# Optimization experiments

Hardware: AMD Instinct MI355X
Metric: run time of the kernel (lower is better)

Reference implementation:

```python
import jax, jax.numpy as jnp
import numpy as np

N_A, N_P = 100000, 150000
N = N_A + N_P          # total nodes in concatenated feature matrix
D = 128                # emb_dim == hidden
C = 16                 # num_classes
E = 2000000            # nnz per relation


def setup_inputs() -> dict:
    key = jax.random.key(0)
    ks = jax.random.split(key, 16)
    s = 1.0 / np.sqrt(D)
    # coefficients as in init_coe: uniform(-b, b) then L1-normalized, coe_num = 1+2+2 = 5
    bound = np.sqrt(3.0 / 5)
    coe_np = np.random.RandomState(0).uniform(-bound, bound, 5)
    coe_np = coe_np / np.sum(np.abs(coe_np))
    return {
        "x0": jax.random.normal(ks[0], (N_A, D), jnp.float32),
        "x1": jax.random.normal(ks[1], (N_P, D), jnp.float32),
        "vals_ap": jax.random.uniform(ks[2], (E,), jnp.float32) * 0.01,
        "vals_pa": jax.random.uniform(ks[3], (E,), jnp.float32) * 0.01,
        # AP: rows are A nodes [0, N_A), cols are P nodes [N_A, N)
        "rows_ap": jax.random.randint(ks[4], (E,), 0, N_A, jnp.int32),
        "cols_ap": jax.random.randint(ks[5], (E,), N_A, N, jnp.int32),
        # PA: rows are P nodes [N_A, N), cols are A nodes [0, N_A)
        "rows_pa": jax.random.randint(ks[6], (E,), N_A, N, jnp.int32),
        "cols_pa": jax.random.randint(ks[7], (E,), 0, N_A, jnp.int32),
        "Wp0": jax.random.normal(ks[8], (D, D), jnp.float32) * s,
        "Wp1": jax.random.normal(ks[9], (D, D), jnp.float32) * s,
        "W1": jax.random.normal(ks[10], (D, D), jnp.float32) * s,
        "b1": jnp.zeros((D,), jnp.float32),
        "W2": jax.random.normal(ks[11], (D, C), jnp.float32) * s,
        "b2": jnp.zeros((C,), jnp.float32),
        "coe": jnp.asarray(coe_np, jnp.float32),
    }


def _spmm(rows, cols, vals, h):
    # sparse [N,N] @ dense [N,D] via gather + segment-sum
    return jax.ops.segment_sum(vals[:, None] * h[cols], rows, num_segments=N)


def _normalize(x):
    mean = x.mean(axis=1, keepdims=True)
    std = jnp.std(x, axis=1, keepdims=True, ddof=1)  # torch std is unbiased
    z = (x - mean) / std
    return jnp.where(jnp.isnan(z), 0.0, z)


def _power_pass(x, coe, ap, pa, first_order):
    # first_order: tuple of relation names in hop-1 order ("AP","PA") or ("PA","AP")
    rel = {"AP": ap, "PA": pa}
    res = coe[0] * x
    h = {}
    for ci, r in enumerate(first_order):
        h[r] = _spmm(*rel[r], x)
        res = res + coe[1 + ci] * h[r]
    # hop 2: compose relation j[:2] with previous result j[2:]
    second = [r + first_order[1 - i] for i, r in enumerate(first_order)]
    for ci, j in enumerate(second):
        out = _spmm(*rel[j[:2]], h[j[2:]])
        res = res + coe[3 + ci] * out
    return res


def reference(x0, x1, vals_ap, vals_pa, rows_ap, cols_ap, rows_pa, cols_pa,
              Wp0, Wp1, W1, b1, W2, b2, coe):
    ap = (rows_ap, cols_ap, vals_ap)
    pa = (rows_pa, cols_pa, vals_pa)
    # per-type projection then concat along node axis
    x = jnp.concatenate([x0 @ Wp0, x1 @ Wp1], axis=0)  # [N, D]
    x = jax.nn.relu(x @ W1 + b1)
    x = _normalize(x)
    # pass 1: lis = {1: [AP, PA], 2: [APPA, PAAP]}
    x = _power_pass(x, coe, ap, pa, ("AP", "PA"))
    # pass 2 (transposed series): lis_t = {1: [PA, AP], 2: [PAAP, APPA]}
    res = _power_pass(x, coe, ap, pa, ("PA", "AP"))
    return res @ W2 + b2  # [N, C]
```

## Files before the change

### kernel.cpp

```cpp
#include <hip/hip_runtime.h>
#include <hip/hip_bf16.h>


typedef float f32x2 __attribute__((ext_vector_type(2)));
typedef float f32x4 __attribute__((ext_vector_type(4)));
typedef short bf16x8 __attribute__((ext_vector_type(8)));

__device__ inline unsigned short f2bf(float x) {
    unsigned b = __float_as_uint(x);
    unsigned r = (b + 0x7fffu + ((b >> 16) & 1u)) >> 16;
    return (unsigned short)r;
}
__device__ inline float bflo(unsigned u) { return __uint_as_float(u << 16); }
__device__ inline float bfhi(unsigned u) { return __uint_as_float(u & 0xffff0000u); }

__device__ inline unsigned pk_fp8x4(float a, float b, float c, float d) {
    int v = __builtin_amdgcn_cvt_pk_fp8_f32(a, b, 0, false);
    v = __builtin_amdgcn_cvt_pk_fp8_f32(c, d, v, true);
    return (unsigned)v;
}

__global__ __launch_bounds__(128) void fuse_w(const float* __restrict__ Wp0,
                                              const float* __restrict__ Wp1,
                                              const float* __restrict__ W1,
                                              unsigned short* __restrict__ Mt0,
                                              unsigned short* __restrict__ Mt1) {
    int m = blockIdx.x >> 7;
    int i = blockIdx.x & 127;
    const float* Wp = m ? Wp1 : Wp0;
    unsigned short* Mt = m ? Mt1 : Mt0;
    __shared__ float r[128];
    int t = threadIdx.x;
    r[t] = Wp[i * 128 + t];
    __syncthreads();
    float acc = 0.f;
    #pragma unroll 8
    for (int k = 0; k < 128; ++k) acc += r[k] * W1[k * 128 + t];
    Mt[t * 128 + i] = f2bf(acc);
}

__global__ __launch_bounds__(256) void gemm_relu_norm(const float* __restrict__ xin,
                                                      const unsigned short* __restrict__ Mt,
                                                      const float* __restrict__ b1,
                                                      unsigned short* __restrict__ xbf,
                                                      unsigned char* __restrict__ x8,
                                                      int nrows) {
    __shared__ char xsh[64 * 256];
    __shared__ char xsl[64 * 256];
    __shared__ char mts[128 * 256];
    int t = threadIdx.x;
    long row0 = (long)blockIdx.x * 64;
    int rows_this = nrows - (int)row0;
    if (rows_this > 64) rows_this = 64;

    #pragma unroll
    for (int it = 0; it < 4; ++it) {
        int idx = it * 256 + t;
        int row = idx >> 4, slot = idx & 15;
        float4 v0 = {0.f, 0.f, 0.f, 0.f}, v1 = {0.f, 0.f, 0.f, 0.f};
        if (row < rows_this) {
            v0 = *(const float4*)(xin + (row0 + row) * 128 + slot * 8);
            v1 = *(const float4*)(xin + (row0 + row) * 128 + slot * 8 + 4);
        }
        float vv[8] = {v0.x, v0.y, v0.z, v0.w, v1.x, v1.y, v1.z, v1.w};
        unsigned hw[8], lw[8];
        #pragma unroll
        for (int j = 0; j < 8; ++j) {
            unsigned h = f2bf(vv[j]);
            float hv = __uint_as_float(h << 16);
            hw[j] = h;
            lw[j] = f2bf(vv[j] - hv);
        }
        uint4 ph, pl;
        ph.x = hw[0] | (hw[1] << 16); ph.y = hw[2] | (hw[3] << 16);
        ph.z = hw[4] | (hw[5] << 16); ph.w = hw[6] | (hw[7] << 16);
        pl.x = lw[0] | (lw[1] << 16); pl.y = lw[2] | (lw[3] << 16);
        pl.z = lw[4] | (lw[5] << 16); pl.w = lw[6] | (lw[7] << 16);
        int off = row * 256 + ((slot ^ (row & 7)) << 4);
        *(uint4*)&xsh[off] = ph;
        *(uint4*)&xsl[off] = pl;
    }
    #pragma unroll
    for (int it = 0; it < 8; ++it) {
        int idx = it * 256 + t;
        int row = idx >> 4, slot = idx & 15;
        uint4 mv = ((const uint4*)Mt)[idx];
        *(uint4*)&mts[row * 256 + ((slot ^ (row & 7)) << 4)] = mv;
    }
    __syncthreads();

    int w = t >> 6;
    int lidx = t & 15;
    int grp = (t >> 4) & 3;
    f32x4 acc[8];
    #pragma unroll
    for (int nt = 0; nt < 8; ++nt) acc[nt] = (f32x4){0.f, 0.f, 0.f, 0.f};

    #pragma unroll
    for (int ks = 0; ks < 4; ++ks) {
        int arow = w * 16 + lidx;
        int slot = ks * 4 + grp;
        bf16x8 ah = *(bf16x8*)&xsh[arow * 256 + ((slot ^ (arow & 7)) << 4)];
        bf16x8 al = *(bf16x8*)&xsl[arow * 256 + ((slot ^ (arow & 7)) << 4)];
        #pragma unroll
        for (int nt = 0; nt < 8; ++nt) {
            int brow = nt * 16 + lidx;
            bf16x8 bb = *(bf16x8*)&mts[brow * 256 + ((slot ^ (brow & 7)) << 4)];
            acc[nt] = __builtin_amdgcn_mfma_f32_16x16x32_bf16(al, bb, acc[nt], 0, 0, 0);
            acc[nt] = __builtin_amdgcn_mfma_f32_16x16x32_bf16(ah, bb, acc[nt], 0, 0, 0);
        }
    }

    float bias[8];
    #pragma unroll
    for (int nt = 0; nt < 8; ++nt) bias[nt] = b1[nt * 16 + lidx];

    #pragma unroll
    for (int r = 0; r < 4; ++r) {
        int row_loc = w * 16 + grp * 4 + r;
        float v[8];
        float s = 0.f;
        #pragma unroll
        for (int nt = 0; nt < 8; ++nt) {
            float x = acc[nt][r] + bias[nt];
            x = x > 0.f ? x : 0.f;
            v[nt] = x;
            s += x;
        }
        s += __shfl_xor(s, 1); s += __shfl_xor(s, 2);
        s += __shfl_xor(s, 4); s += __shfl_xor(s, 8);
        float mean = s * (1.0f / 128.0f);
        float q = 0.f;
        #pragma unroll
        for (int nt = 0; nt < 8; ++nt) {
            float d = v[nt] - mean;
            v[nt] = d;
            q += d * d;
        }
        q += __shfl_xor(q, 1); q += __shfl_xor(q, 2);
        q += __shfl_xor(q, 4); q += __shfl_xor(q, 8);
        float inv = 0.f;
        if (q > 0.f) inv = 1.0f / sqrtf(q * (1.0f / 127.0f));
        #pragma unroll
        for (int nt = 0; nt < 8; ++nt)
            *(unsigned short*)&xsh[row_loc * 256 + (nt * 16 + lidx) * 2] = f2bf(v[nt] * inv);
    }
    __syncthreads();

    #pragma unroll
    for (int it = 0; it < 4; ++it) {
        int idx = it * 256 + t;
        int row = idx >> 4, slot = idx & 15;
        if (row < rows_this) {
            uint4 zv = *(uint4*)&xsh[row * 256 + slot * 16];
            *(uint4*)(xbf + (row0 + row) * 128 + slot * 8) = zv;
            uint2 p8;
            p8.x = pk_fp8x4(bflo(zv.x), bfhi(zv.x), bflo(zv.y), bfhi(zv.y));
            p8.y = pk_fp8x4(bflo(zv.z), bfhi(zv.z), bflo(zv.w), bfhi(zv.w));
            *(uint2*)(x8 + (row0 + row) * 128 + slot * 8) = p8;
        }
    }
}

__global__ __launch_bounds__(256) void count_rows(const int* __restrict__ rows, int E,
                                                  int* __restrict__ cnt) {
    int i = (blockIdx.x * 256 + threadIdx.x) * 4;
    if (i + 4 <= E) {
        int4 r = *(const int4*)(rows + i);
        atomicAdd(&cnt[r.x], 1);
        atomicAdd(&cnt[r.y], 1);
        atomicAdd(&cnt[r.z], 1);
        atomicAdd(&cnt[r.w], 1);
    } else {
        for (; i < E; ++i) atomicAdd(&cnt[rows[i]], 1);
    }
}

__global__ __launch_bounds__(256) void scan1(const int* __restrict__ cnt, int R,
                                             int* __restrict__ rp, int* __restrict__ bt) {
    __shared__ int lds[256];
    int t = threadIdx.x, b = blockIdx.x;
    int base = b * 4096 + t * 16;
    int v[16];
    int s = 0;
    #pragma unroll
    for (int i = 0; i < 16; ++i) {
        int idx = base + i;
        int c = (idx < R) ? cnt[idx] : 0;
        v[i] = s;
        s += c;
    }
    lds[t] = s;
    __syncthreads();
    for (int off = 1; off < 256; off <<= 1) {
        int x = (t >= off) ? lds[t - off] : 0;
        __syncthreads();
        lds[t] += x;
        __syncthreads();
    }
    int excl = lds[t] - s;
    #pragma unroll
    for (int i = 0; i < 16; ++i) {
        int idx = base + i;
        if (idx < R) rp[idx] = excl + v[i];
    }
    if (t == 0) bt[b] = lds[255];
}

__global__ __launch_bounds__(64) void scan2(const int* __restrict__ bt, int B,
                                            int* __restrict__ bo, int* __restrict__ rp,
                                            int R, int E2) {
    int t = threadIdx.x;
    int v = (t < B) ? bt[t] : 0;
    int inc = v;
    #pragma unroll
    for (int off = 1; off < 64; off <<= 1) {
        int y = __shfl_up(inc, off);
        if (t >= off) inc += y;
    }
    if (t < B) bo[t] = inc - v;
    if (t == 0) rp[R] = E2;
}

__global__ __launch_bounds__(256) void scan3(int* __restrict__ rp, const int* __restrict__ bo,
                                             int R) {
    int i = blockIdx.x * 256 + threadIdx.x;
    if (i < R) rp[i] = rp[i] + bo[i >> 12];
}

__global__ __launch_bounds__(256) void binit(const int* __restrict__ rp, int NR,
                                             int nbuck, int* __restrict__ bcur) {
    int b = blockIdx.x * 256 + threadIdx.x;
    if (b < nbuck) {
        int r = b << 9;
        if (r > NR) r = NR;
        bcur[b] = rp[r];
    }
}

__global__ __launch_bounds__(256) void partition_edges(const int* __restrict__ rows,
                                                       const int* __restrict__ cols,
                                                       const float* __restrict__ vals,
                                                       int E, int nbuck,
                                                       int* __restrict__ bcur,
                                                       int2* __restrict__ tmp) {
    __shared__ int hist[512];
    __shared__ int gbase[512];
    __shared__ int cnt2[512];
    int t = threadIdx.x;
    for (int b = t; b < nbuck; b += 256) { hist[b] = 0; cnt2[b] = 0; }
    __syncthreads();
    long base = (long)blockIdx.x * 4096;
    #pragma unroll
    for (int k = 0; k < 16; ++k) {
        long i = base + k * 256 + t;
        if (i < E) atomicAdd(&hist[rows[i] >> 9], 1);
    }
    __syncthreads();
    for (int b = t; b < nbuck; b += 256) {
        int h = hist[b];
        gbase[b] = h ? atomicAdd(&bcur[b], h) : 0;
    }
    __syncthreads();
    #pragma unroll
    for (int k = 0; k < 16; ++k) {
        long i = base + k * 256 + t;
        if (i < E) {
            int rl = rows[i];
            int b = rl >> 9;
            int rank = atomicAdd(&cnt2[b], 1);
            int2 rec;
            rec.x = ((rl - (b << 9)) << 18) | cols[i];
            rec.y = __float_as_int(vals[i]);
            tmp[gbase[b] + rank] = rec;
        }
    }
}

__global__ __launch_bounds__(1024) void place_edges(const int* __restrict__ rp,
                                                    const int2* __restrict__ tmp,
                                                    int NR,
                                                    int2* __restrict__ scv) {
    __shared__ int hist[512];
    __shared__ int hoff[512];
    int b = blockIdx.x;
    int srow = b << 9;
    int erow = srow + 512;
    if (erow > NR) erow = NR;
    int start = rp[srow], endp = rp[erow];
    int t = threadIdx.x;
    if (t < 512) hist[t] = 0;
    __syncthreads();

    for (int i = start + t; i < endp; i += 1024)
        atomicAdd(&hist[tmp[i].x >> 18], 1);
    __syncthreads();

    if (t < 512) hoff[t] = hist[t];
    __syncthreads();
    for (int off = 1; off < 512; off <<= 1) {
        int v = 0;
        if (t < 512 && t >= off) v = hoff[t - off];
        __syncthreads();
        if (t < 512) hoff[t] += v;
        __syncthreads();
    }
    if (t < 512) hoff[t] = start + hoff[t] - hist[t];
    __syncthreads();

    int i = start + t;
    for (; i + 3 * 1024 < endp; i += 4 * 1024) {
        int2 a0 = tmp[i];
        int2 a1 = tmp[i + 1024];
        int2 a2 = tmp[i + 2048];
        int2 a3 = tmp[i + 3072];
        int p0 = atomicAdd(&hoff[a0.x >> 18], 1);
        int p1 = atomicAdd(&hoff[a1.x >> 18], 1);
        int p2 = atomicAdd(&hoff[a2.x >> 18], 1);
        int p3 = atomicAdd(&hoff[a3.x >> 18], 1);
        int2 o0; o0.x = a0.x & 0x3ffff; o0.y = a0.y;
        int2 o1; o1.x = a1.x & 0x3ffff; o1.y = a1.y;
        int2 o2; o2.x = a2.x & 0x3ffff; o2.y = a2.y;
        int2 o3; o3.x = a3.x & 0x3ffff; o3.y = a3.y;
        scv[p0] = o0;
        scv[p1] = o1;
        scv[p2] = o2;
        scv[p3] = o3;
    }
    for (; i < endp; i += 1024) {
        int2 rec = tmp[i];
        int p = atomicAdd(&hoff[rec.x >> 18], 1);
        int2 o;
        o.x = rec.x & 0x3ffff;
        o.y = rec.y;
        scv[p] = o;
    }
}

#define DEC_FMA(qq, vv) do {                                                        \
    f32x2 vp_ = {(vv), (vv)};                                                       \
    acc[0] = __builtin_elementwise_fma(vp_, __builtin_amdgcn_cvt_pk_f32_fp8((qq).x, false), acc[0]); \
    acc[1] = __builtin_elementwise_fma(vp_, __builtin_amdgcn_cvt_pk_f32_fp8((qq).x, true),  acc[1]); \
    acc[2] = __builtin_elementwise_fma(vp_, __builtin_amdgcn_cvt_pk_f32_fp8((qq).y, false), acc[2]); \
    acc[3] = __builtin_elementwise_fma(vp_, __builtin_amdgcn_cvt_pk_f32_fp8((qq).y, true),  acc[3]); \
} while (0)

__device__ inline void spmm_core8(const int* __restrict__ rp,
                                  const int2* __restrict__ scv,
                                  const unsigned char* __restrict__ g8,
                                  int row, int f, f32x2* acc) {
    int beg = rp[row], end = rp[row + 1];
    int j = beg;
    if ((j & 1) && j < end) {
        int2 r0 = scv[j];
        uint2 q0 = *(const uint2*)(g8 + ((long)r0.x << 7) + f);
        float v0 = __int_as_float(r0.y);
        DEC_FMA(q0, v0);
        ++j;
    }
    for (; j + 8 <= end; j += 8) {
        int4 s01 = *(const int4*)(scv + j);
        int4 s23 = *(const int4*)(scv + j + 2);
        int4 s45 = *(const int4*)(scv + j + 4);
        int4 s67 = *(const int4*)(scv + j + 6);
        uint2 q0 = *(const uint2*)(g8 + ((long)s01.x << 7) + f);
        uint2 q1 = *(const uint2*)(g8 + ((long)s01.z << 7) + f);
        uint2 q2 = *(const uint2*)(g8 + ((long)s23.x << 7) + f);
        uint2 q3 = *(const uint2*)(g8 + ((long)s23.z << 7) + f);
        uint2 q4 = *(const uint2*)(g8 + ((long)s45.x << 7) + f);
        uint2 q5 = *(const uint2*)(g8 + ((long)s45.z << 7) + f);
        uint2 q6 = *(const uint2*)(g8 + ((long)s67.x << 7) + f);
        uint2 q7 = *(const uint2*)(g8 + ((long)s67.z << 7) + f);
        DEC_FMA(q0, __int_as_float(s01.y));
        DEC_FMA(q1, __int_as_float(s01.w));
        DEC_FMA(q2, __int_as_float(s23.y));
        DEC_FMA(q3, __int_as_float(s23.w));
        DEC_FMA(q4, __int_as_float(s45.y));
        DEC_FMA(q5, __int_as_float(s45.w));
        DEC_FMA(q6, __int_as_float(s67.y));
        DEC_FMA(q7, __int_as_float(s67.w));
    }
    for (; j + 2 <= end; j += 2) {
        int4 s01 = *(const int4*)(scv + j);
        uint2 q0 = *(const uint2*)(g8 + ((long)s01.x << 7) + f);
        uint2 q1 = *(const uint2*)(g8 + ((long)s01.z << 7) + f);
        DEC_FMA(q0, __int_as_float(s01.y));
        DEC_FMA(q1, __int_as_float(s01.w));
    }
    if (j < end) {
        int2 r0 = scv[j];
        uint2 q0 = *(const uint2*)(g8 + ((long)r0.x << 7) + f);
        float v0 = __int_as_float(r0.y);
        DEC_FMA(q0, v0);
    }
}

__global__ __launch_bounds__(256) void spmm_plain(const int* __restrict__ rp,
                                                  const int2* __restrict__ scv,
                                                  const unsigned char* __restrict__ x8,
                                                  unsigned short* __restrict__ houtbf,
                                                  unsigned char* __restrict__ hout8,
                                                  int R) {
    int wave = blockIdx.x * 4 + (threadIdx.x >> 6);
    int lane = threadIdx.x & 63;
    int row = wave * 4 + (lane >> 4);
    if (row >= R) return;
    int f = (lane & 15) << 3;
    f32x2 acc[4];
    #pragma unroll
    for (int i = 0; i < 4; ++i) acc[i] = (f32x2){0.f, 0.f};
    spmm_core8(rp, scv, x8, row, f, acc);
    uint4 o;
    o.x = (unsigned)f2bf(acc[0].x) | ((unsigned)f2bf(acc[0].y) << 16);
    o.y = (unsigned)f2bf(acc[1].x) | ((unsigned)f2bf(acc[1].y) << 16);
    o.z = (unsigned)f2bf(acc[2].x) | ((unsigned)f2bf(acc[2].y) << 16);
    o.w = (unsigned)f2bf(acc[3].x) | ((unsigned)f2bf(acc[3].y) << 16);
    *(uint4*)(houtbf + ((long)row << 7) + f) = o;
    uint2 o8;
    o8.x = pk_fp8x4(acc[0].x, acc[0].y, acc[1].x, acc[1].y);
    o8.y = pk_fp8x4(acc[2].x, acc[2].y, acc[3].x, acc[3].y);
    *(uint2*)(hout8 + ((long)row << 7) + f) = o8;
}

__global__ __launch_bounds__(256) void spmm_update(const int* __restrict__ rp,
                                                   const int2* __restrict__ scv,
                                                   const unsigned char* __restrict__ h8,
                                                   const unsigned short* __restrict__ hbf,
                                                   unsigned short* __restrict__ Xbf,
                                                   unsigned char* __restrict__ X8,
                                                   const float* __restrict__ coe,
                                                   int ihA, int iaA, int ihP, int iaP,
                                                   int NA, int R) {
    int wave = blockIdx.x * 4 + (threadIdx.x >> 6);
    int lane = threadIdx.x & 63;
    int row = wave * 4 + (lane >> 4);
    if (row >= R) return;
    int f = (lane & 15) << 3;
    f32x2 acc[4];
    #pragma unroll
    for (int i = 0; i < 4; ++i) acc[i] = (f32x2){0.f, 0.f};
    spmm_core8(rp, scv, h8, row, f, acc);

    float c0 = coe[0];
    float ch = coe[row < NA ? ihA : ihP];
    float ca = coe[row < NA ? iaA : iaP];
    long o = ((long)row << 7) + f;
    uint4 xv = *(const uint4*)(Xbf + o);
    uint4 hs = *(const uint4*)(hbf + o);
    float r[8];
    r[0] = c0 * bflo(xv.x) + ch * bflo(hs.x) + ca * acc[0].x;
    r[1] = c0 * bfhi(xv.x) + ch * bfhi(hs.x) + ca * acc[0].y;
    r[2] = c0 * bflo(xv.y) + ch * bflo(hs.y) + ca * acc[1].x;
    r[3] = c0 * bfhi(xv.y) + ch * bfhi(hs.y) + ca * acc[1].y;
    r[4] = c0 * bflo(xv.z) + ch * bflo(hs.z) + ca * acc[2].x;
    r[5] = c0 * bfhi(xv.z) + ch * bfhi(hs.z) + ca * acc[2].y;
    r[6] = c0 * bflo(xv.w) + ch * bflo(hs.w) + ca * acc[3].x;
    r[7] = c0 * bfhi(xv.w) + ch * bfhi(hs.w) + ca * acc[3].y;
    uint4 ob;
    ob.x = (unsigned)f2bf(r[0]) | ((unsigned)f2bf(r[1]) << 16);
    ob.y = (unsigned)f2bf(r[2]) | ((unsigned)f2bf(r[3]) << 16);
    ob.z = (unsigned)f2bf(r[4]) | ((unsigned)f2bf(r[5]) << 16);
    ob.w = (unsigned)f2bf(r[6]) | ((unsigned)f2bf(r[7]) << 16);
    *(uint4*)(Xbf + o) = ob;
    uint2 o8;
    o8.x = pk_fp8x4(r[0], r[1], r[2], r[3]);
    o8.y = pk_fp8x4(r[4], r[5], r[6], r[7]);
    *(uint2*)(X8 + o) = o8;
}

__global__ __launch_bounds__(256) void spmm_update_out(const int* __restrict__ rp,
                                                       const int2* __restrict__ scv,
                                                       const unsigned char* __restrict__ h8,
                                                       const unsigned short* __restrict__ hbf,
                                                       const unsigned short* __restrict__ Xbf,
                                                       const float* __restrict__ coe,
                                                       const float* __restrict__ W2,
                                                       const float* __restrict__ b2,
                                                       float* __restrict__ out,
                                                       int ihA, int iaA, int ihP, int iaP,
                                                       int NA, int R) {
    __shared__ float xs[16 * 132];
    __shared__ float wT[16 * 132];
    __shared__ float bs[16];
    int t = threadIdx.x;
    #pragma unroll
    for (int i = 0; i < 8; ++i) {
        int idx = i * 256 + t;
        wT[(idx & 15) * 132 + (idx >> 4)] = W2[idx];
    }
    if (t < 16) bs[t] = b2[t];

    int lane = t & 63;
    int rl = (t >> 6) * 4 + (lane >> 4);
    int row = blockIdx.x * 16 + rl;
    int f = (lane & 15) << 3;
    if (row < R) {
        f32x2 acc[4];
        #pragma unroll
        for (int i = 0; i < 4; ++i) acc[i] = (f32x2){0.f, 0.f};
        spmm_core8(rp, scv, h8, row, f, acc);
        float c0 = coe[0];
        float ch = coe[row < NA ? ihA : ihP];
        float ca = coe[row < NA ? iaA : iaP];
        long o = ((long)row << 7) + f;
        uint4 xv = *(const uint4*)(Xbf + o);
        uint4 hs = *(const uint4*)(hbf + o);
        float* x = &xs[rl * 132 + f];
        x[0] = c0 * bflo(xv.x) + ch * bflo(hs.x) + ca * acc[0].x;
        x[1] = c0 * bfhi(xv.x) + ch * bfhi(hs.x) + ca * acc[0].y;
        x[2] = c0 * bflo(xv.y) + ch * bflo(hs.y) + ca * acc[1].x;
        x[3] = c0 * bfhi(xv.y) + ch * bfhi(hs.y) + ca * acc[1].y;
        x[4] = c0 * bflo(xv.z) + ch * bflo(hs.z) + ca * acc[2].x;
        x[5] = c0 * bfhi(xv.z) + ch * bfhi(hs.z) + ca * acc[2].y;
        x[6] = c0 * bflo(xv.w) + ch * bflo(hs.w) + ca * acc[3].x;
        x[7] = c0 * bfhi(xv.w) + ch * bfhi(hs.w) + ca * acc[3].y;
    }
    __syncthreads();
    int orl = t >> 4, c = t & 15;
    long orow = (long)blockIdx.x * 16 + orl;
    if (orow < R) {
        const float* xrow = &xs[orl * 132];
        const float* wrow = &wT[c * 132];
        f32x4 a4 = {0.f, 0.f, 0.f, 0.f};
        #pragma unroll 8
        for (int k = 0; k < 128; k += 4) {
            f32x4 xv = *(const f32x4*)(xrow + k);
            f32x4 wv = *(const f32x4*)(wrow + k);
            a4 = __builtin_elementwise_fma(xv, wv, a4);
        }
        out[orow * 16 + c] = a4.x + a4.y + a4.z + a4.w + bs[c];
    }
}

extern "C" void kernel_launch(void* const* d_in, const int* in_sizes, int n_in,
                              void* d_out, int out_size, void* d_ws, size_t ws_size,
                              hipStream_t stream) {
    const float* x0  = (const float*)d_in[0];
    const float* x1  = (const float*)d_in[1];
    const float* vap = (const float*)d_in[2];
    const float* vpa = (const float*)d_in[3];
    const int*   rap = (const int*)d_in[4];
    const int*   cap = (const int*)d_in[5];
    const int*   rpa = (const int*)d_in[6];
    const int*   cpa = (const int*)d_in[7];
    const float* Wp0 = (const float*)d_in[8];
    const float* Wp1 = (const float*)d_in[9];
    const float* W1  = (const float*)d_in[10];
    const float* b1  = (const float*)d_in[11];
    const float* W2  = (const float*)d_in[12];
    const float* b2  = (const float*)d_in[13];
    const float* coe = (const float*)d_in[14];
    float* out = (float*)d_out;

    const int NA = in_sizes[0] / 128;
    const int NP = in_sizes[1] / 128;
    const int N  = NA + NP;
    const int E  = in_sizes[2];
    const int E2 = 2 * E;

    char* p = (char*)d_ws;
    auto alloc = [&](size_t bytes) {
        char* r = p;
        p += (bytes + 255) & ~(size_t)255;
        return r;
    };
    unsigned short* Xbf = (unsigned short*)alloc((size_t)N * 128 * 2);
    unsigned short* hbf = (unsigned short*)alloc((size_t)N * 128 * 2);
    unsigned char* X8 = (unsigned char*)alloc((size_t)N * 128);
    unsigned char* h8 = (unsigned char*)alloc((size_t)N * 128);
    unsigned short* Mt0 = (unsigned short*)alloc(128 * 128 * 2);
    unsigned short* Mt1 = (unsigned short*)alloc(128 * 128 * 2);
    int* cnt   = (int*)alloc((size_t)N * 4);
    int* rp    = (int*)alloc((size_t)(N + 1) * 4);
    int* bt    = (int*)alloc(64 * 4);
    int* bo    = (int*)alloc(64 * 4);
    int2* scv  = (int2*)alloc((size_t)E2 * 8);
    int* bcur  = (int*)alloc(512 * 4);
    if ((size_t)(p - (char*)d_ws) > ws_size) return;

    int2* tmp = (int2*)Xbf;

    const int nbuck = (N + 511) >> 9;
    const int pg = (E + 4095) / 4096;

    hipMemsetAsync(cnt, 0, (size_t)N * 4, stream);
    const int cg = (E / 4 + 255) / 256;
    count_rows<<<cg, 256, 0, stream>>>(rap, E, cnt);
    count_rows<<<cg, 256, 0, stream>>>(rpa, E, cnt);
    int B = (N + 4095) / 4096;
    scan1<<<B, 256, 0, stream>>>(cnt, N, rp, bt);
    scan2<<<1, 64, 0, stream>>>(bt, B, bo, rp, N, E2);
    scan3<<<(N + 255) / 256, 256, 0, stream>>>(rp, bo, N);
    binit<<<2, 256, 0, stream>>>(rp, N, nbuck, bcur);
    partition_edges<<<pg, 256, 0, stream>>>(rap, cap, vap, E, nbuck, bcur, tmp);
    partition_edges<<<pg, 256, 0, stream>>>(rpa, cpa, vpa, E, nbuck, bcur, tmp);
    place_edges<<<nbuck, 1024, 0, stream>>>(rp, tmp, N, scv);

    fuse_w<<<256, 128, 0, stream>>>(Wp0, Wp1, W1, Mt0, Mt1);
    gemm_relu_norm<<<(NA + 63) / 64, 256, 0, stream>>>(x0, Mt0, b1, Xbf, X8, NA);
    gemm_relu_norm<<<(NP + 63) / 64, 256, 0, stream>>>(
        x1, Mt1, b1, Xbf + (size_t)NA * 128, X8 + (size_t)NA * 128, NP);

    const int sg = (N + 15) / 16;

    spmm_plain<<<sg, 256, 0, stream>>>(rp, scv, X8, hbf, h8, N);
    spmm_update<<<sg, 256, 0, stream>>>(rp, scv, h8, hbf, Xbf, X8, coe, 1, 3, 2, 4, NA, N);

    spmm_plain<<<sg, 256, 0, stream>>>(rp, scv, X8, hbf, h8, N);
    spmm_update_out<<<sg, 256, 0, stream>>>(rp, scv, h8, hbf, Xbf, coe,
                                            W2, b2, out, 2, 4, 1, 3, NA, N);
}
```

Baseline: 913.4 us.

## Assign one wavefront per row in SpMM, splitting edges across quarter-waves

The SpMM kernels switch from four rows per wavefront (16 lanes each) to one row per wavefront. Each quarter-wave handles every fourth pair of edges, and the partial sums are combined with cross-lane shuffles. The goal is more memory-level parallelism per row and better load balance across rows of uneven degree, which matters at an average of about 16 edges per row. In exchange, three quarters of the lanes sit idle during the epilogue, and padding edges are masked by zeroing their values, which needs a zeroed tail on the edge array to keep over-reads safe.

```diff
diff --git a/kernel.cpp b/kernel.cpp
--- a/kernel.cpp
+++ b/kernel.cpp
@@ -345,53 +345,39 @@
     acc[3] = __builtin_elementwise_fma(vp_, __builtin_amdgcn_cvt_pk_f32_fp8((qq).y, true),  acc[3]); \
 } while (0)
 
-__device__ inline void spmm_core8(const int* __restrict__ rp,
-                                  const int2* __restrict__ scv,
-                                  const unsigned char* __restrict__ g8,
-                                  int row, int f, f32x2* acc) {
-    int beg = rp[row], end = rp[row + 1];
-    int j = beg;
-    if ((j & 1) && j < end) {
-        int2 r0 = scv[j];
-        uint2 q0 = *(const uint2*)(g8 + ((long)r0.x << 7) + f);
-        float v0 = __int_as_float(r0.y);
-        DEC_FMA(q0, v0);
-        ++j;
-    }
-    for (; j + 8 <= end; j += 8) {
-        int4 s01 = *(const int4*)(scv + j);
-        int4 s23 = *(const int4*)(scv + j + 2);
-        int4 s45 = *(const int4*)(scv + j + 4);
-        int4 s67 = *(const int4*)(scv + j + 6);
-        uint2 q0 = *(const uint2*)(g8 + ((long)s01.x << 7) + f);
-        uint2 q1 = *(const uint2*)(g8 + ((long)s01.z << 7) + f);
-        uint2 q2 = *(const uint2*)(g8 + ((long)s23.x << 7) + f);
-        uint2 q3 = *(const uint2*)(g8 + ((long)s23.z << 7) + f);
-        uint2 q4 = *(const uint2*)(g8 + ((long)s45.x << 7) + f);
-        uint2 q5 = *(const uint2*)(g8 + ((long)s45.z << 7) + f);
-        uint2 q6 = *(const uint2*)(g8 + ((long)s67.x << 7) + f);
-        uint2 q7 = *(const uint2*)(g8 + ((long)s67.z << 7) + f);
-        DEC_FMA(q0, __int_as_float(s01.y));
-        DEC_FMA(q1, __int_as_float(s01.w));
-        DEC_FMA(q2, __int_as_float(s23.y));
-        DEC_FMA(q3, __int_as_float(s23.w));
-        DEC_FMA(q4, __int_as_float(s45.y));
-        DEC_FMA(q5, __int_as_float(s45.w));
-        DEC_FMA(q6, __int_as_float(s67.y));
-        DEC_FMA(q7, __int_as_float(s67.w));
-    }
-    for (; j + 2 <= end; j += 2) {
-        int4 s01 = *(const int4*)(scv + j);
-        uint2 q0 = *(const uint2*)(g8 + ((long)s01.x << 7) + f);
-        uint2 q1 = *(const uint2*)(g8 + ((long)s01.z << 7) + f);
-        DEC_FMA(q0, __int_as_float(s01.y));
-        DEC_FMA(q1, __int_as_float(s01.w));
-    }
-    if (j < end) {
-        int2 r0 = scv[j];
-        uint2 q0 = *(const uint2*)(g8 + ((long)r0.x << 7) + f);
-        float v0 = __int_as_float(r0.y);
-        DEC_FMA(q0, v0);
+__device__ inline void spmm_row8(const int2* __restrict__ scv,
+                                 const unsigned char* __restrict__ g8,
+                                 int beg, int end, int q2, int f, bool kf,
+                                 f32x2* acc) {
+    int base = beg & ~1;
+    int nst = (end - base + 7) >> 3;
+    int b = base;
+    for (int s = 0; s < nst; ++s, b += 8) {
+        int4 sv = *(const int4*)(scv + b + q2);
+        float v0 = __int_as_float(sv.y);
+        float v1 = __int_as_float(sv.w);
+        if (s == 0) {
+            if (kf) v0 = 0.f;
+        }
+        if (s == nst - 1) {
+            int rem = end - b;
+            if (q2 >= rem) v0 = 0.f;
+            if (q2 + 1 >= rem) v1 = 0.f;
+        }
+        uint2 g0 = *(const uint2*)(g8 + ((long)sv.x << 7) + f);
+        uint2 g1 = *(const uint2*)(g8 + ((long)sv.z << 7) + f);
+        DEC_FMA(g0, v0);
+        DEC_FMA(g1, v1);
+    }
+}
+
+__device__ inline void qreduce(f32x2* acc) {
+    #pragma unroll
+    for (int i = 0; i < 4; ++i) {
+        acc[i].x += __shfl_xor(acc[i].x, 16);
+        acc[i].y += __shfl_xor(acc[i].y, 16);
+        acc[i].x += __shfl_xor(acc[i].x, 32);
+        acc[i].y += __shfl_xor(acc[i].y, 32);
     }
 }
 
@@ -401,25 +387,30 @@
                                                   unsigned short* __restrict__ houtbf,
                                                   unsigned char* __restrict__ hout8,
                                                   int R) {
-    int wave = blockIdx.x * 4 + (threadIdx.x >> 6);
+    int row = blockIdx.x * 4 + (threadIdx.x >> 6);
+    if (row >= R) return;
     int lane = threadIdx.x & 63;
-    int row = wave * 4 + (lane >> 4);
-    if (row >= R) return;
-    int f = (lane & 15) << 3;
+    int q = lane >> 4, f = (lane & 15) << 3;
+    int beg = rp[row], end = rp[row + 1];
     f32x2 acc[4];
     #pragma unroll
     for (int i = 0; i < 4; ++i) acc[i] = (f32x2){0.f, 0.f};
-    spmm_core8(rp, scv, x8, row, f, acc);
-    uint4 o;
-    o.x = (unsigned)f2bf(acc[0].x) | ((unsigned)f2bf(acc[0].y) << 16);
-    o.y = (unsigned)f2bf(acc[1].x) | ((unsigned)f2bf(acc[1].y) << 16);
-    o.z = (unsigned)f2bf(acc[2].x) | ((unsigned)f2bf(acc[2].y) << 16);
-    o.w = (unsigned)f2bf(acc[3].x) | ((unsigned)f2bf(acc[3].y) << 16);
-    *(uint4*)(houtbf + ((long)row << 7) + f) = o;
-    uint2 o8;
-    o8.x = pk_fp8x4(acc[0].x, acc[0].y, acc[1].x, acc[1].y);
-    o8.y = pk_fp8x4(acc[2].x, acc[2].y, acc[3].x, acc[3].y);
-    *(uint2*)(hout8 + ((long)row << 7) + f) = o8;
+    spmm_row8(scv, x8, beg, end, q * 2, f, (beg & 1) && (q == 0), acc);
+    qreduce(acc);
+    long o = ((long)row << 7) + f;
+    if (q == 0) {
+        uint4 ob;
+        ob.x = (unsigned)f2bf(acc[0].x) | ((unsigned)f2bf(acc[0].y) << 16);
+        ob.y = (unsigned)f2bf(acc[1].x) | ((unsigned)f2bf(acc[1].y) << 16);
+        ob.z = (unsigned)f2bf(acc[2].x) | ((unsigned)f2bf(acc[2].y) << 16);
+        ob.w = (unsigned)f2bf(acc[3].x) | ((unsigned)f2bf(acc[3].y) << 16);
+        *(uint4*)(houtbf + o) = ob;
+    } else if (q == 1) {
+        uint2 o8;
+        o8.x = pk_fp8x4(acc[0].x, acc[0].y, acc[1].x, acc[1].y);
+        o8.y = pk_fp8x4(acc[2].x, acc[2].y, acc[3].x, acc[3].y);
+        *(uint2*)(hout8 + o) = o8;
+    }
 }
 
 __global__ __launch_bounds__(256) void spmm_update(const int* __restrict__ rp,
@@ -431,104 +422,116 @@
                                                    const float* __restrict__ coe,
                                                    int ihA, int iaA, int ihP, int iaP,
                                                    int NA, int R) {
-    int wave = blockIdx.x * 4 + (threadIdx.x >> 6);
+    int row = blockIdx.x * 4 + (threadIdx.x >> 6);
+    if (row >= R) return;
     int lane = threadIdx.x & 63;
-    int row = wave * 4 + (lane >> 4);
-    if (row >= R) return;
-    int f = (lane & 15) << 3;
+    int q = lane >> 4, f = (lane & 15) << 3;
+    int beg = rp[row], end = rp[row + 1];
     f32x2 acc[4];
     #pragma unroll
     for (int i = 0; i < 4; ++i) acc[i] = (f32x2){0.f, 0.f};
-    spmm_core8(rp, scv, h8, row, f, acc);
-
-    float c0 = coe[0];
-    float ch = coe[row < NA ? ihA : ihP];
-    float ca = coe[row < NA ? iaA : iaP];
-    long o = ((long)row << 7) + f;
-    uint4 xv = *(const uint4*)(Xbf + o);
-    uint4 hs = *(const uint4*)(hbf + o);
-    float r[8];
-    r[0] = c0 * bflo(xv.x) + ch * bflo(hs.x) + ca * acc[0].x;
-    r[1] = c0 * bfhi(xv.x) + ch * bfhi(hs.x) + ca * acc[0].y;
-    r[2] = c0 * bflo(xv.y) + ch * bflo(hs.y) + ca * acc[1].x;
-    r[3] = c0 * bfhi(xv.y) + ch * bfhi(hs.y) + ca * acc[1].y;
-    r[4] = c0 * bflo(xv.z) + ch * bflo(hs.z) + ca * acc[2].x;
-    r[5] = c0 * bfhi(xv.z) + ch * bfhi(hs.z) + ca * acc[2].y;
-    r[6] = c0 * bflo(xv.w) + ch * bflo(hs.w) + ca * acc[3].x;
-    r[7] = c0 * bfhi(xv.w) + ch * bfhi(hs.w) + ca * acc[3].y;
-    uint4 ob;
-    ob.x = (unsigned)f2bf(r[0]) | ((unsigned)f2bf(r[1]) << 16);
-    ob.y = (unsigned)f2bf(r[2]) | ((unsigned)f2bf(r[3]) << 16);
-    ob.z = (unsigned)f2bf(r[4]) | ((unsigned)f2bf(r[5]) << 16);
-    ob.w = (unsigned)f2bf(r[6]) | ((unsigned)f2bf(r[7]) << 16);
-    *(uint4*)(Xbf + o) = ob;
-    uint2 o8;
-    o8.x = pk_fp8x4(r[0], r[1], r[2], r[3]);
-    o8.y = pk_fp8x4(r[4], r[5], r[6], r[7]);
-    *(uint2*)(X8 + o) = o8;
-}
-
-__global__ __launch_bounds__(256) void spmm_update_out(const int* __restrict__ rp,
-                                                       const int2* __restrict__ scv,
-                                                       const unsigned char* __restrict__ h8,
-                                                       const unsigned short* __restrict__ hbf,
-                                                       const unsigned short* __restrict__ Xbf,
-                                                       const float* __restrict__ coe,
-                                                       const float* __restrict__ W2,
-                                                       const float* __restrict__ b2,
-                                                       float* __restrict__ out,
-                                                       int ihA, int iaA, int ihP, int iaP,
-                                                       int NA, int R) {
-    __shared__ float xs[16 * 132];
-    __shared__ float wT[16 * 132];
-    __shared__ float bs[16];
-    int t = threadIdx.x;
-    #pragma unroll
-    for (int i = 0; i < 8; ++i) {
-        int idx = i * 256 + t;
-        wT[(idx & 15) * 132 + (idx >> 4)] = W2[idx];
-    }
-    if (t < 16) bs[t] = b2[t];
-
-    int lane = t & 63;
-    int rl = (t >> 6) * 4 + (lane >> 4);
-    int row = blockIdx.x * 16 + rl;
-    int f = (lane & 15) << 3;
-    if (row < R) {
-        f32x2 acc[4];
-        #pragma unroll
-        for (int i = 0; i < 4; ++i) acc[i] = (f32x2){0.f, 0.f};
-        spmm_core8(rp, scv, h8, row, f, acc);
+    spmm_row8(scv, h8, beg, end, q * 2, f, (beg & 1) && (q == 0), acc);
+    qreduce(acc);
+
+    if (q < 2) {
         float c0 = coe[0];
         float ch = coe[row < NA ? ihA : ihP];
         float ca = coe[row < NA ? iaA : iaP];
         long o = ((long)row << 7) + f;
         uint4 xv = *(const uint4*)(Xbf + o);
         uint4 hs = *(const uint4*)(hbf + o);
-        float* x = &xs[rl * 132 + f];
-        x[0] = c0 * bflo(xv.x) + ch * bflo(hs.x) + ca * acc[0].x;
-        x[1] = c0 * bfhi(xv.x) + ch * bfhi(hs.x) + ca * acc[0].y;
-        x[2] = c0 * bflo(xv.y) + ch * bflo(hs.y) + ca * acc[1].x;
-        x[3] = c0 * bfhi(xv.y) + ch * bfhi(hs.y) + ca * acc[1].y;
-        x[4] = c0 * bflo(xv.z) + ch * bflo(hs.z) + ca * acc[2].x;
-        x[5] = c0 * bfhi(xv.z) + ch * bfhi(hs.z) + ca * acc[2].y;
-        x[6] = c0 * bflo(xv.w) + ch * bflo(hs.w) + ca * acc[3].x;
-        x[7] = c0 * bfhi(xv.w) + ch * bfhi(hs.w) + ca * acc[3].y;
-    }
-    __syncthreads();
-    int orl = t >> 4, c = t & 15;
-    long orow = (long)blockIdx.x * 16 + orl;
-    if (orow < R) {
-        const float* xrow = &xs[orl * 132];
-        const float* wrow = &wT[c * 132];
-        f32x4 a4 = {0.f, 0.f, 0.f, 0.f};
-        #pragma unroll 8
-        for (int k = 0; k < 128; k += 4) {
-            f32x4 xv = *(const f32x4*)(xrow + k);
-            f32x4 wv = *(const f32x4*)(wrow + k);
-            a4 = __builtin_elementwise_fma(xv, wv, a4);
-        }
-        out[orow * 16 + c] = a4.x + a4.y + a4.z + a4.w + bs[c];
+        float r[8];
+        r[0] = c0 * bflo(xv.x) + ch * bflo(hs.x) + ca * acc[0].x;
+        r[1] = c0 * bfhi(xv.x) + ch * bfhi(hs.x) + ca * acc[0].y;
+        r[2] = c0 * bflo(xv.y) + ch * bflo(hs.y) + ca * acc[1].x;
+        r[3] = c0 * bfhi(xv.y) + ch * bfhi(hs.y) + ca * acc[1].y;
+        r[4] = c0 * bflo(xv.z) + ch * bflo(hs.z) + ca * acc[2].x;
+        r[5] = c0 * bfhi(xv.z) + ch * bfhi(hs.z) + ca * acc[2].y;
+        r[6] = c0 * bflo(xv.w) + ch * bflo(hs.w) + ca * acc[3].x;
+        r[7] = c0 * bfhi(xv.w) + ch * bfhi(hs.w) + ca * acc[3].y;
+        if (q == 0) {
+            uint4 ob;
+            ob.x = (unsigned)f2bf(r[0]) | ((unsigned)f2bf(r[1]) << 16);
+            ob.y = (unsigned)f2bf(r[2]) | ((unsigned)f2bf(r[3]) << 16);
+            ob.z = (unsigned)f2bf(r[4]) | ((unsigned)f2bf(r[5]) << 16);
+            ob.w = (unsigned)f2bf(r[6]) | ((unsigned)f2bf(r[7]) << 16);
+            *(uint4*)(Xbf + o) = ob;
+        } else {
+            uint2 o8;
+            o8.x = pk_fp8x4(r[0], r[1], r[2], r[3]);
+            o8.y = pk_fp8x4(r[4], r[5], r[6], r[7]);
+            *(uint2*)(X8 + o) = o8;
+        }
+    }
+}
+
+__global__ __launch_bounds__(1024) void spmm_update_out(const int* __restrict__ rp,
+                                                        const int2* __restrict__ scv,
+                                                        const unsigned char* __restrict__ h8,
+                                                        const unsigned short* __restrict__ hbf,
+                                                        const unsigned short* __restrict__ Xbf,
+                                                        const float* __restrict__ coe,
+                                                        const float* __restrict__ W2,
+                                                        const float* __restrict__ b2,
+                                                        float* __restrict__ out,
+                                                        int ihA, int iaA, int ihP, int iaP,
+                                                        int NA, int R) {
+    __shared__ float xs[16 * 132];
+    __shared__ float wT[16 * 132];
+    __shared__ float bs[16];
+    int t = threadIdx.x;
+    #pragma unroll
+    for (int i = 0; i < 2; ++i) {
+        int idx = i * 1024 + t;
+        wT[(idx & 15) * 132 + (idx >> 4)] = W2[idx];
+    }
+    if (t < 16) bs[t] = b2[t];
+
+    int wv = t >> 6;
+    int row = blockIdx.x * 16 + wv;
+    int lane = t & 63;
+    int q = lane >> 4, f = (lane & 15) << 3;
+    if (row < R) {
+        int beg = rp[row], end = rp[row + 1];
+        f32x2 acc[4];
+        #pragma unroll
+        for (int i = 0; i < 4; ++i) acc[i] = (f32x2){0.f, 0.f};
+        spmm_row8(scv, h8, beg, end, q * 2, f, (beg & 1) && (q == 0), acc);
+        qreduce(acc);
+        if (q == 0) {
+            float c0 = coe[0];
+            float ch = coe[row < NA ? ihA : ihP];
+            float ca = coe[row < NA ? iaA : iaP];
+            long o = ((long)row << 7) + f;
+            uint4 xv = *(const uint4*)(Xbf + o);
+            uint4 hs = *(const uint4*)(hbf + o);
+            float* x = &xs[wv * 132 + f];
+            x[0] = c0 * bflo(xv.x) + ch * bflo(hs.x) + ca * acc[0].x;
+            x[1] = c0 * bfhi(xv.x) + ch * bfhi(hs.x) + ca * acc[0].y;
+            x[2] = c0 * bflo(xv.y) + ch * bflo(hs.y) + ca * acc[1].x;
+            x[3] = c0 * bfhi(xv.y) + ch * bfhi(hs.y) + ca * acc[1].y;
+            x[4] = c0 * bflo(xv.z) + ch * bflo(hs.z) + ca * acc[2].x;
+            x[5] = c0 * bfhi(xv.z) + ch * bfhi(hs.z) + ca * acc[2].y;
+            x[6] = c0 * bflo(xv.w) + ch * bflo(hs.w) + ca * acc[3].x;
+            x[7] = c0 * bfhi(xv.w) + ch * bfhi(hs.w) + ca * acc[3].y;
+        }
+    }
+    __syncthreads();
+    if (t < 256) {
+        int orl = t >> 4, c = t & 15;
+        long orow = (long)blockIdx.x * 16 + orl;
+        if (orow < R) {
+            const float* xrow = &xs[orl * 132];
+            const float* wrow = &wT[c * 132];
+            f32x4 a4 = {0.f, 0.f, 0.f, 0.f};
+            #pragma unroll 8
+            for (int k = 0; k < 128; k += 4) {
+                f32x4 xv = *(const f32x4*)(xrow + k);
+                f32x4 wv2 = *(const f32x4*)(wrow + k);
+                a4 = __builtin_elementwise_fma(xv, wv2, a4);
+            }
+            out[orow * 16 + c] = a4.x + a4.y + a4.z + a4.w + bs[c];
+        }
     }
 }
 
@@ -574,7 +577,7 @@
     int* rp    = (int*)alloc((size_t)(N + 1) * 4);
     int* bt    = (int*)alloc(64 * 4);
     int* bo    = (int*)alloc(64 * 4);
-    int2* scv  = (int2*)alloc((size_t)E2 * 8);
+    int2* scv  = (int2*)alloc(((size_t)E2 + 8) * 8);
     int* bcur  = (int*)alloc(512 * 4);
     if ((size_t)(p - (char*)d_ws) > ws_size) return;
 
@@ -584,6 +587,7 @@
     const int pg = (E + 4095) / 4096;
 
     hipMemsetAsync(cnt, 0, (size_t)N * 4, stream);
+    hipMemsetAsync(scv + E2, 0, 8 * sizeof(int2), stream);
     const int cg = (E / 4 + 255) / 256;
     count_rows<<<cg, 256, 0, stream>>>(rap, E, cnt);
     count_rows<<<cg, 256, 0, stream>>>(rpa, E, cnt);
@@ -601,12 +605,13 @@
     gemm_relu_norm<<<(NP + 63) / 64, 256, 0, stream>>>(
         x1, Mt1, b1, Xbf + (size_t)NA * 128, X8 + (size_t)NA * 128, NP);
 
-    const int sg = (N + 15) / 16;
-
-    spmm_plain<<<sg, 256, 0, stream>>>(rp, scv, X8, hbf, h8, N);
-    spmm_update<<<sg, 256, 0, stream>>>(rp, scv, h8, hbf, Xbf, X8, coe, 1, 3, 2, 4, NA, N);
-
-    spmm_plain<<<sg, 256, 0, stream>>>(rp, scv, X8, hbf, h8, N);
-    spmm_update_out<<<sg, 256, 0, stream>>>(rp, scv, h8, hbf, Xbf, coe,
-                                            W2, b2, out, 2, 4, 1, 3, NA, N);
-}
+    const int sg4  = (N + 3) / 4;
+    const int sg16 = (N + 15) / 16;
+
+    spmm_plain<<<sg4, 256, 0, stream>>>(rp, scv, X8, hbf, h8, N);
+    spmm_update<<<sg4, 256, 0, stream>>>(rp, scv, h8, hbf, Xbf, X8, coe, 1, 3, 2, 4, NA, N);
+
+    spmm_plain<<<sg4, 256, 0, stream>>>(rp, scv, X8, hbf, h8, N);
+    spmm_update_out<<<sg16, 1024, 0, stream>>>(rp, scv, h8, hbf, Xbf, coe,
+                                               W2, b2, out, 2, 4, 1, 3, NA, N);
+}
```

New measurement: 1.062 ms. +16.3%, slower.

## Sort rows by degree so SpMM waves process rows of similar length

Applied to the files above, without the earlier changes.

Adds a counting-sort pass (histogram, scan, scatter) that builds a row permutation grouped by row degree, capped at 63. The SpMM kernels then index rows through this order, so the four rows sharing a wave have similar nonzero counts, which is meant to reduce lane divergence and idle time within a wave. In exchange it adds three small kernels, an extra indirection per row, and scattered output writes instead of contiguous ones. It also pads scv with zeroed entries.

```diff
diff --git a/kernel.cpp b/kernel.cpp
--- a/kernel.cpp
+++ b/kernel.cpp
@@ -235,6 +235,57 @@
         int r = b << 9;
         if (r > NR) r = NR;
         bcur[b] = rp[r];
+    }
+}
+
+__global__ __launch_bounds__(256) void dhist(const int* __restrict__ rp, int R,
+                                             int* __restrict__ dcnt) {
+    __shared__ int h[64];
+    int t = threadIdx.x;
+    if (t < 64) h[t] = 0;
+    __syncthreads();
+    int i = blockIdx.x * 256 + t;
+    if (i < R) {
+        int d = rp[i + 1] - rp[i];
+        if (d > 63) d = 63;
+        atomicAdd(&h[d], 1);
+    }
+    __syncthreads();
+    if (t < 64 && h[t]) atomicAdd(&dcnt[t], h[t]);
+}
+
+__global__ __launch_bounds__(64) void dscan(int* __restrict__ dcnt) {
+    int t = threadIdx.x;
+    int v = dcnt[t];
+    int inc = v;
+    #pragma unroll
+    for (int off = 1; off < 64; off <<= 1) {
+        int y = __shfl_up(inc, off);
+        if (t >= off) inc += y;
+    }
+    dcnt[t] = inc - v;
+}
+
+__global__ __launch_bounds__(256) void dscatter(const int* __restrict__ rp, int R,
+                                                int* __restrict__ dcur,
+                                                int* __restrict__ order) {
+    __shared__ int h[64], gb[64], c2[64];
+    int t = threadIdx.x;
+    if (t < 64) { h[t] = 0; c2[t] = 0; }
+    __syncthreads();
+    int i = blockIdx.x * 256 + t;
+    int d = 0;
+    if (i < R) {
+        d = rp[i + 1] - rp[i];
+        if (d > 63) d = 63;
+        atomicAdd(&h[d], 1);
+    }
+    __syncthreads();
+    if (t < 64) gb[t] = h[t] ? atomicAdd(&dcur[t], h[t]) : 0;
+    __syncthreads();
+    if (i < R) {
+        int r = atomicAdd(&c2[d], 1);
+        order[gb[d] + r] = i;
     }
 }
 
@@ -398,43 +449,46 @@
 __global__ __launch_bounds__(256) void spmm_plain(const int* __restrict__ rp,
                                                   const int2* __restrict__ scv,
                                                   const unsigned char* __restrict__ x8,
+                                                  const int* __restrict__ order,
                                                   unsigned short* __restrict__ houtbf,
                                                   unsigned char* __restrict__ hout8,
                                                   int R) {
-    int wave = blockIdx.x * 4 + (threadIdx.x >> 6);
+    int qi = blockIdx.x * 16 + (threadIdx.x >> 4);
+    if (qi >= R) return;
+    int row = order[qi];
     int lane = threadIdx.x & 63;
-    int row = wave * 4 + (lane >> 4);
-    if (row >= R) return;
     int f = (lane & 15) << 3;
     f32x2 acc[4];
     #pragma unroll
     for (int i = 0; i < 4; ++i) acc[i] = (f32x2){0.f, 0.f};
     spmm_core8(rp, scv, x8, row, f, acc);
-    uint4 o;
-    o.x = (unsigned)f2bf(acc[0].x) | ((unsigned)f2bf(acc[0].y) << 16);
-    o.y = (unsigned)f2bf(acc[1].x) | ((unsigned)f2bf(acc[1].y) << 16);
-    o.z = (unsigned)f2bf(acc[2].x) | ((unsigned)f2bf(acc[2].y) << 16);
-    o.w = (unsigned)f2bf(acc[3].x) | ((unsigned)f2bf(acc[3].y) << 16);
-    *(uint4*)(houtbf + ((long)row << 7) + f) = o;
+    long o = ((long)row << 7) + f;
+    uint4 ob;
+    ob.x = (unsigned)f2bf(acc[0].x) | ((unsigned)f2bf(acc[0].y) << 16);
+    ob.y = (unsigned)f2bf(acc[1].x) | ((unsigned)f2bf(acc[1].y) << 16);
+    ob.z = (unsigned)f2bf(acc[2].x) | ((unsigned)f2bf(acc[2].y) << 16);
+    ob.w = (unsigned)f2bf(acc[3].x) | ((unsigned)f2bf(acc[3].y) << 16);
+    *(uint4*)(houtbf + o) = ob;
     uint2 o8;
     o8.x = pk_fp8x4(acc[0].x, acc[0].y, acc[1].x, acc[1].y);
     o8.y = pk_fp8x4(acc[2].x, acc[2].y, acc[3].x, acc[3].y);
-    *(uint2*)(hout8 + ((long)row << 7) + f) = o8;
+    *(uint2*)(hout8 + o) = o8;
 }
 
 __global__ __launch_bounds__(256) void spmm_update(const int* __restrict__ rp,
                                                    const int2* __restrict__ scv,
                                                    const unsigned char* __restrict__ h8,
                                                    const unsigned short* __restrict__ hbf,
+                                                   const int* __restrict__ order,
                                                    unsigned short* __restrict__ Xbf,
                                                    unsigned char* __restrict__ X8,
                                                    const float* __restrict__ coe,
                                                    int ihA, int iaA, int ihP, int iaP,
                                                    int NA, int R) {
-    int wave = blockIdx.x * 4 + (threadIdx.x >> 6);
+    int qi = blockIdx.x * 16 + (threadIdx.x >> 4);
+    if (qi >= R) return;
+    int row = order[qi];
     int lane = threadIdx.x & 63;
-    int row = wave * 4 + (lane >> 4);
-    if (row >= R) return;
     int f = (lane & 15) << 3;
     f32x2 acc[4];
     #pragma unroll
@@ -473,6 +527,7 @@
                                                        const unsigned char* __restrict__ h8,
                                                        const unsigned short* __restrict__ hbf,
                                                        const unsigned short* __restrict__ Xbf,
+                                                       const int* __restrict__ order,
                                                        const float* __restrict__ coe,
                                                        const float* __restrict__ W2,
                                                        const float* __restrict__ b2,
@@ -490,11 +545,12 @@
     }
     if (t < 16) bs[t] = b2[t];
 
+    int rl = t >> 4;
+    int qi = blockIdx.x * 16 + rl;
     int lane = t & 63;
-    int rl = (t >> 6) * 4 + (lane >> 4);
-    int row = blockIdx.x * 16 + rl;
     int f = (lane & 15) << 3;
-    if (row < R) {
+    if (qi < R) {
+        int row = order[qi];
         f32x2 acc[4];
         #pragma unroll
         for (int i = 0; i < 4; ++i) acc[i] = (f32x2){0.f, 0.f};
@@ -517,8 +573,9 @@
     }
     __syncthreads();
     int orl = t >> 4, c = t & 15;
-    long orow = (long)blockIdx.x * 16 + orl;
-    if (orow < R) {
+    int oqi = blockIdx.x * 16 + orl;
+    if (oqi < R) {
+        long orow = order[oqi];
         const float* xrow = &xs[orl * 132];
         const float* wrow = &wT[c * 132];
         f32x4 a4 = {0.f, 0.f, 0.f, 0.f};
@@ -572,9 +629,11 @@
     unsigned short* Mt1 = (unsigned short*)alloc(128 * 128 * 2);
     int* cnt   = (int*)alloc((size_t)N * 4);
     int* rp    = (int*)alloc((size_t)(N + 1) * 4);
+    int* order = (int*)alloc((size_t)N * 4);
+    int* dcnt  = (int*)alloc(64 * 4);
     int* bt    = (int*)alloc(64 * 4);
     int* bo    = (int*)alloc(64 * 4);
-    int2* scv  = (int2*)alloc((size_t)E2 * 8);
+    int2* scv  = (int2*)alloc(((size_t)E2 + 8) * 8);
     int* bcur  = (int*)alloc(512 * 4);
     if ((size_t)(p - (char*)d_ws) > ws_size) return;
 
@@ -582,16 +641,24 @@
 
     const int nbuck = (N + 511) >> 9;
     const int pg = (E + 4095) / 4096;
+    const int ng = (N + 255) / 256;
 
     hipMemsetAsync(cnt, 0, (size_t)N * 4, stream);
+    hipMemsetAsync(dcnt, 0, 64 * 4, stream);
+    hipMemsetAsync(scv + E2, 0, 8 * sizeof(int2), stream);
     const int cg = (E / 4 + 255) / 256;
     count_rows<<<cg, 256, 0, stream>>>(rap, E, cnt);
     count_rows<<<cg, 256, 0, stream>>>(rpa, E, cnt);
     int B = (N + 4095) / 4096;
     scan1<<<B, 256, 0, stream>>>(cnt, N, rp, bt);
     scan2<<<1, 64, 0, stream>>>(bt, B, bo, rp, N, E2);
-    scan3<<<(N + 255) / 256, 256, 0, stream>>>(rp, bo, N);
+    scan3<<<ng, 256, 0, stream>>>(rp, bo, N);
     binit<<<2, 256, 0, stream>>>(rp, N, nbuck, bcur);
+
+    dhist<<<ng, 256, 0, stream>>>(rp, N, dcnt);
+    dscan<<<1, 64, 0, stream>>>(dcnt);
+    dscatter<<<ng, 256, 0, stream>>>(rp, N, dcnt, order);
+
     partition_edges<<<pg, 256, 0, stream>>>(rap, cap, vap, E, nbuck, bcur, tmp);
     partition_edges<<<pg, 256, 0, stream>>>(rpa, cpa, vpa, E, nbuck, bcur, tmp);
     place_edges<<<nbuck, 1024, 0, stream>>>(rp, tmp, N, scv);
@@ -603,10 +670,11 @@
 
     const int sg = (N + 15) / 16;
 
-    spmm_plain<<<sg, 256, 0, stream>>>(rp, scv, X8, hbf, h8, N);
-    spmm_update<<<sg, 256, 0, stream>>>(rp, scv, h8, hbf, Xbf, X8, coe, 1, 3, 2, 4, NA, N);
-
-    spmm_plain<<<sg, 256, 0, stream>>>(rp, scv, X8, hbf, h8, N);
-    spmm_update_out<<<sg, 256, 0, stream>>>(rp, scv, h8, hbf, Xbf, coe,
+    spmm_plain<<<sg, 256, 0, stream>>>(rp, scv, X8, order, hbf, h8, N);
+    spmm_update<<<sg, 256, 0, stream>>>(rp, scv, h8, hbf, order, Xbf, X8, coe,
+                                        1, 3, 2, 4, NA, N);
+
+    spmm_plain<<<sg, 256, 0, stream>>>(rp, scv, X8, order, hbf, h8, N);
+    spmm_update_out<<<sg, 256, 0, stream>>>(rp, scv, h8, hbf, Xbf, order, coe,
                                             W2, b2, out, 2, 4, 1, 3, NA, N);
 }
```

New measurement: 978.5 us. 1.07x slower.
